# Kernel tuning notes

Hardware: AMD Instinct MI355X
Metric: run time of the kernel (lower is better)

Reference implementation:

```python
import jax, jax.numpy as jnp
import numpy as np

COMMITMENT_COST = 0.25


def setup_inputs() -> dict:
    key = jax.random.key(0)
    k1, k2 = jax.random.split(key)
    x = jax.random.normal(k1, (32, 256, 32, 32), dtype=jnp.float32)          # NCHW latents
    embedding = jax.random.normal(k2, (1024, 256), dtype=jnp.float32)        # [K, D] codebook
    return {"x": x, "embedding": embedding}


def reference(x, embedding):
    # NCHW -> NHWC, flatten to [N, D]
    inp = jnp.transpose(x, (0, 2, 3, 1))
    B, H, W, D = inp.shape
    K = embedding.shape[0]
    flat = inp.reshape(-1, D)                                                # [N, D]

    dists = (jnp.sum(flat * flat, axis=1, keepdims=True)
             + jnp.sum(embedding * embedding, axis=1)
             - 2.0 * flat @ embedding.T)
    idx = jnp.argmin(dists, axis=1)                                          # [N]
    encodings = jax.nn.one_hot(idx, K, dtype=flat.dtype)                     # [N, K]

    quantized = (encodings @ embedding).reshape(B, H, W, D)

    # commitment loss (codebook detached, eval path: no EMA update)
    e_latent_loss = jnp.mean(jnp.square(jax.lax.stop_gradient(quantized) - inp))
    loss = COMMITMENT_COST * e_latent_loss

    # straight-through estimator
    quantized_st = inp + jax.lax.stop_gradient(quantized - inp)

    avg_probs = jnp.mean(encodings, axis=0)
    perplexity = jnp.exp(-jnp.sum(avg_probs * jnp.log(avg_probs + 1e-10)))

    return (loss, jnp.transpose(quantized_st, (0, 3, 1, 2)), perplexity, encodings)
```

## Files before the change

### kernel.cpp

```cpp
#include <hip/hip_runtime.h>
#include <math.h>

#define D    256
#define K    1024
#define HWX  1024
#define NPTS 32768
#define PT   64
#define NPAIR 32

#define Q_OFF    1
#define PERP_OFF (1 + 8388608)
#define ENC_OFF  (2 + 8388608)

#define WS_FRAG_OFF 16384

typedef __attribute__((ext_vector_type(8))) short bf16x8;
typedef __attribute__((ext_vector_type(4))) float f32x4;

__device__ __forceinline__ unsigned short bf16_rne(float f) {
  unsigned int u = __float_as_uint(f);
  u = u + 0x7fffu + ((u >> 16) & 1u);
  return (unsigned short)(u >> 16);
}

#define CONV(F, H, L)                                                          \
  {                                                                            \
    H = bf16_rne(F);                                                           \
    const float fh_ = __uint_as_float((unsigned)(H) << 16);                    \
    L = bf16_rne((F)-fh_);                                                     \
  }

__global__ __launch_bounds__(256) void vq_frag(const float* __restrict__ emb,
                                               unsigned int* __restrict__ frag,
                                               float* __restrict__ enorm,
                                               int* __restrict__ counts,
                                               float* __restrict__ loss_accum) {
  const int gid = blockIdx.x * 256 + threadIdx.x;
  const int c = gid >> 5, g = gid & 31;
  const float* src = emb + (size_t)c * D + g * 8;
  const float4 a = *(const float4*)src;
  const float4 b = *(const float4*)(src + 4);
  float s = a.x * a.x + a.y * a.y + a.z * a.z + a.w * a.w +
            b.x * b.x + b.y * b.y + b.z * b.z + b.w * b.w;
#pragma unroll
  for (int off = 1; off < 32; off <<= 1) s += __shfl_xor(s, off);
  if (g == 0) enorm[c] = s;
  unsigned short h0, h1, h2, h3, h4, h5, h6, h7;
  unsigned short l0, l1, l2, l3, l4, l5, l6, l7;
  CONV(a.x, h0, l0) CONV(a.y, h1, l1) CONV(a.z, h2, l2) CONV(a.w, h3, l3)
  CONV(b.x, h4, l4) CONV(b.y, h5, l5) CONV(b.z, h6, l6) CONV(b.w, h7, l7)
  uint4 uh, ul;
  uh.x = (unsigned)h0 | ((unsigned)h1 << 16); uh.y = (unsigned)h2 | ((unsigned)h3 << 16);
  uh.z = (unsigned)h4 | ((unsigned)h5 << 16); uh.w = (unsigned)h6 | ((unsigned)h7 << 16);
  ul.x = (unsigned)l0 | ((unsigned)l1 << 16); ul.y = (unsigned)l2 | ((unsigned)l3 << 16);
  ul.z = (unsigned)l4 | ((unsigned)l5 << 16); ul.w = (unsigned)l6 | ((unsigned)l7 << 16);
  const int fragidx = (c >> 4) * 16 + (g >> 2) * 2;
  const int Lo = ((c & 15) + 16 * (g & 3)) * 4;
  *(uint4*)(frag + (size_t)fragidx * 256 + Lo) = uh;
  *(uint4*)(frag + (size_t)(fragidx + 1) * 256 + Lo) = ul;
  if (gid < K) counts[gid] = 0;
  if (gid == 0) *loss_accum = 0.0f;
}

#define ISSUE_PAIR(P, SEL)                                                     \
  {                                                                            \
    const unsigned* gsrc = fragg + (((size_t)(P)*32 + w * 8) * 256) + lane * 4; \
    unsigned short* ldst = fbuf + (SEL)*16384 + (w * 8) * 512;                 \
    _Pragma("unroll") for (int q = 0; q < 8; ++q)                              \
        __builtin_amdgcn_global_load_lds(                                      \
            (const __attribute__((address_space(1))) unsigned*)(gsrc + q * 256), \
            (__attribute__((address_space(3))) unsigned*)(ldst + q * 512),     \
            16, 0, 0);                                                         \
  }

#define AH(RTL, KS)                                                            \
  ah##RTL##_##KS = *(const bf16x8*)&fbuf[(((pg * 2 + RTL) * 8 + KS) * 2 + 0) * 512 + lane * 8]; \
  al##RTL##_##KS = *(const bf16x8*)&fbuf[(((pg * 2 + RTL) * 8 + KS) * 2 + 1) * 512 + lane * 8];

#define KS(KSv)                                                                \
  {                                                                            \
    const bf16x8 bh = *(const bf16x8*)&fbuf[bufo + (KSv * 2 + 0) * 512 + lane * 8]; \
    const bf16x8 bl = *(const bf16x8*)&fbuf[bufo + (KSv * 2 + 1) * 512 + lane * 8]; \
    acc0 = __builtin_amdgcn_mfma_f32_16x16x32_bf16(ah0_##KSv, bh, acc0, 0, 0, 0); \
    acc0 = __builtin_amdgcn_mfma_f32_16x16x32_bf16(al0_##KSv, bh, acc0, 0, 0, 0); \
    acc0 = __builtin_amdgcn_mfma_f32_16x16x32_bf16(ah0_##KSv, bl, acc0, 0, 0, 0); \
    acc0 = __builtin_amdgcn_mfma_f32_16x16x32_bf16(al0_##KSv, bl, acc0, 0, 0, 0); \
    acc1 = __builtin_amdgcn_mfma_f32_16x16x32_bf16(ah1_##KSv, bh, acc1, 0, 0, 0); \
    acc1 = __builtin_amdgcn_mfma_f32_16x16x32_bf16(al1_##KSv, bh, acc1, 0, 0, 0); \
    acc1 = __builtin_amdgcn_mfma_f32_16x16x32_bf16(ah1_##KSv, bl, acc1, 0, 0, 0); \
    acc1 = __builtin_amdgcn_mfma_f32_16x16x32_bf16(al1_##KSv, bl, acc1, 0, 0, 0); \
  }

__global__ __launch_bounds__(256) void vq_main(const float* __restrict__ x,
                                               const unsigned int* __restrict__ fragg,
                                               const float* __restrict__ emb,
                                               const float* __restrict__ enorm,
                                               float* __restrict__ out_q,
                                               float* __restrict__ out_enc,
                                               float* __restrict__ loss_accum,
                                               int* __restrict__ counts) {
  __shared__ __align__(16) unsigned short fbuf[32768];
  __shared__ float en_s[K];
  __shared__ float xn_part[256];
  __shared__ float red_val[128];
  __shared__ int red_idx[128];
  __shared__ int idx_s[PT];

  const int t = threadIdx.x;
  const int lane = t & 63;
  const int w = t >> 6;
  const int pg = w >> 1;
  const int par = w & 1;
  const int p0 = blockIdx.x * PT;
  const int bb = p0 >> 10;
  const int hw0 = p0 & 1023;

  {
    const int pt = t & 63, c0 = t >> 6;
    const int rt = pt >> 4, mrow = pt & 15;
    const float* xb = x + (size_t)bb * (D * HWX) + hw0 + pt;
    float xn = 0.0f;
    for (int c = c0; c < D; c += 4) {
      const float f = xb[(size_t)c * HWX];
      unsigned short h, l;
      CONV(f, h, l)
      xn += f * f;
      const int ks = c >> 5, quad = (c >> 3) & 3, j = c & 7;
      const int Lr = mrow + 16 * quad;
      fbuf[((rt * 8 + ks) * 2 + 0) * 512 + Lr * 8 + j] = h;
      fbuf[((rt * 8 + ks) * 2 + 1) * 512 + Lr * 8 + j] = l;
    }
    xn_part[t] = xn;
  }
  for (int i = t; i < K; i += 256) en_s[i] = enorm[i];
  __syncthreads();

  bf16x8 ah0_0, ah0_1, ah0_2, ah0_3, ah0_4, ah0_5, ah0_6, ah0_7;
  bf16x8 al0_0, al0_1, al0_2, al0_3, al0_4, al0_5, al0_6, al0_7;
  bf16x8 ah1_0, ah1_1, ah1_2, ah1_3, ah1_4, ah1_5, ah1_6, ah1_7;
  bf16x8 al1_0, al1_1, al1_2, al1_3, al1_4, al1_5, al1_6, al1_7;
  AH(0, 0) AH(0, 1) AH(0, 2) AH(0, 3) AH(0, 4) AH(0, 5) AH(0, 6) AH(0, 7)
  AH(1, 0) AH(1, 1) AH(1, 2) AH(1, 3) AH(1, 4) AH(1, 5) AH(1, 6) AH(1, 7)
  __syncthreads();

  float mv[8];
  int mi[8];
#pragma unroll
  for (int i = 0; i < 8; ++i) { mv[i] = 3.4e38f; mi[i] = 0; }

  ISSUE_PAIR(0, 0)
  int sel = 0;
  for (int p = 0; p < NPAIR; ++p) {
    __syncthreads();
    if (p + 1 < NPAIR) ISSUE_PAIR(p + 1, sel ^ 1)
    const int bufo = sel * 16384 + par * 16 * 512;
    f32x4 acc0 = {0.f, 0.f, 0.f, 0.f};
    f32x4 acc1 = {0.f, 0.f, 0.f, 0.f};
    KS(0) KS(1) KS(2) KS(3) KS(4) KS(5) KS(6) KS(7)
    const int code = (p * 2 + par) * 16 + (lane & 15);
    const float en_l = en_s[code];
    float m;
    m = en_l - 2.0f * acc0[0]; if (m < mv[0]) { mv[0] = m; mi[0] = code; }
    m = en_l - 2.0f * acc0[1]; if (m < mv[1]) { mv[1] = m; mi[1] = code; }
    m = en_l - 2.0f * acc0[2]; if (m < mv[2]) { mv[2] = m; mi[2] = code; }
    m = en_l - 2.0f * acc0[3]; if (m < mv[3]) { mv[3] = m; mi[3] = code; }
    m = en_l - 2.0f * acc1[0]; if (m < mv[4]) { mv[4] = m; mi[4] = code; }
    m = en_l - 2.0f * acc1[1]; if (m < mv[5]) { mv[5] = m; mi[5] = code; }
    m = en_l - 2.0f * acc1[2]; if (m < mv[6]) { mv[6] = m; mi[6] = code; }
    m = en_l - 2.0f * acc1[3]; if (m < mv[7]) { mv[7] = m; mi[7] = code; }
    sel ^= 1;
  }

#pragma unroll
  for (int off = 1; off < 16; off <<= 1) {
#pragma unroll
    for (int i = 0; i < 8; ++i) {
      const float ov = __shfl_xor(mv[i], off);
      const int oi = __shfl_xor(mi[i], off);
      if (ov < mv[i] || (ov == mv[i] && oi < mi[i])) { mv[i] = ov; mi[i] = oi; }
    }
  }
  if ((lane & 15) == 0) {
    const int quad = lane >> 4;
#pragma unroll
    for (int i = 0; i < 8; ++i) {
      const int loc = (i >> 2) * 16 + quad * 4 + (i & 3);
      red_val[w * 32 + loc] = mv[i];
      red_idx[w * 32 + loc] = mi[i];
    }
  }
  __syncthreads();
  float dist = 0.0f;
  if (t < PT) {
    const int pgm = t >> 5, loc = t & 31;
    float bv = red_val[(pgm * 2) * 32 + loc];
    int bi = red_idx[(pgm * 2) * 32 + loc];
    const float v1 = red_val[(pgm * 2 + 1) * 32 + loc];
    const int i1 = red_idx[(pgm * 2 + 1) * 32 + loc];
    if (v1 < bv || (v1 == bv && i1 < bi)) { bv = v1; bi = i1; }
    float xn = 0.0f;
#pragma unroll
    for (int g = 0; g < 4; ++g) xn += xn_part[t + 64 * g];
    dist = bv + xn;
    idx_s[t] = bi;
    atomicAdd(&counts[bi], 1);
  }
  if (t < 64) {
#pragma unroll
    for (int off = 32; off > 0; off >>= 1) dist += __shfl_down(dist, off);
    if (t == 0) atomicAdd(loss_accum, dist);
  }
  __syncthreads();

  {
    const int pt = t & 63, c0 = t >> 6;
    const int row = idx_s[pt];
    const float* er = emb + (size_t)row * D;
    float* qb = out_q + (size_t)bb * D * HWX + hw0 + pt;
#pragma unroll
    for (int c = c0; c < D; c += 4) qb[(size_t)c * HWX] = er[c];
  }
  {
    float2* eb2 = reinterpret_cast<float2*>(out_enc + (size_t)p0 * K);
#pragma unroll 4
    for (int i = t; i < PT * K / 2; i += 256) {
      const int row = i >> 9;
      const int c2 = (i & 511) * 2;
      const int target = idx_s[row];
      float2 v = make_float2(0.f, 0.f);
      if (target == c2) v.x = 1.0f;
      else if (target == c2 + 1) v.y = 1.0f;
      eb2[i] = v;
    }
  }
}

__global__ __launch_bounds__(256) void vq_final(const int* __restrict__ counts,
                                                const float* __restrict__ loss_accum,
                                                float* __restrict__ out) {
  __shared__ float sh[4];
  const int t = threadIdx.x;
  float s = 0.0f;
  for (int k = t; k < K; k += 256) {
    const float p = (float)counts[k] * (1.0f / 32768.0f);
    s += p * logf(p + 1e-10f);
  }
#pragma unroll
  for (int off = 32; off > 0; off >>= 1) s += __shfl_down(s, off);
  if ((t & 63) == 0) sh[t >> 6] = s;
  __syncthreads();
  if (t == 0) {
    const float tot = sh[0] + sh[1] + sh[2] + sh[3];
    out[PERP_OFF] = expf(-tot);
    out[0] = 0.25f * (*loss_accum) / 8388608.0f;
  }
}

extern "C" void kernel_launch(void* const* d_in, const int* in_sizes, int n_in,
                              void* d_out, int out_size, void* d_ws, size_t ws_size,
                              hipStream_t stream) {
  const float* x = (const float*)d_in[0];
  const float* emb = (const float*)d_in[1];
  float* out = (float*)d_out;
  float* enorm = (float*)d_ws;
  int* counts = (int*)((char*)d_ws + 4096);
  float* loss_accum = (float*)((char*)d_ws + 8192);
  unsigned int* fragg = (unsigned int*)((char*)d_ws + WS_FRAG_OFF);

  hipLaunchKernelGGL(vq_frag, dim3(128), dim3(256), 0, stream,
                     emb, fragg, enorm, counts, loss_accum);
  hipLaunchKernelGGL(vq_main, dim3(NPTS / PT), dim3(256), 0, stream,
                     x, fragg, emb, enorm, out + Q_OFF, out + ENC_OFF,
                     loss_accum, counts);
  hipLaunchKernelGGL(vq_final, dim3(1), dim3(256), 0, stream,
                     counts, loss_accum, out);
}
```

Before: 287.7 us.

## Read codebook fragments from global directly, drop lo*lo MFMA, stage quantized output via LDS

The main loop no longer double-buffers codebook fragments into LDS with global_load_lds and barriers. Each wave now reads its B fragments straight from global/L2, and the per-pair __syncthreads calls are gone. The low*low bf16 correction MFMA is dropped, cutting MFMA work by a quarter at a small cost in distance precision that could flip near-tie argmins. The quantized output gather is restaged through LDS with a padded transpose so the embedding row reads are coalesced float4 loads. The workspace fragment offset also moves, possibly to avoid overlap.

Result: slower. 309.1 us (+7.4%).

```diff
diff --git a/kernel.cpp b/kernel.cpp
--- a/kernel.cpp
+++ b/kernel.cpp
@@ -12,7 +12,7 @@
 #define PERP_OFF (1 + 8388608)
 #define ENC_OFF  (2 + 8388608)
 
-#define WS_FRAG_OFF 16384
+#define WS_FRAG_OFF 147456
 
 typedef __attribute__((ext_vector_type(8))) short bf16x8;
 typedef __attribute__((ext_vector_type(4))) float f32x4;
@@ -62,33 +62,20 @@
   if (gid == 0) *loss_accum = 0.0f;
 }
 
-#define ISSUE_PAIR(P, SEL)                                                     \
-  {                                                                            \
-    const unsigned* gsrc = fragg + (((size_t)(P)*32 + w * 8) * 256) + lane * 4; \
-    unsigned short* ldst = fbuf + (SEL)*16384 + (w * 8) * 512;                 \
-    _Pragma("unroll") for (int q = 0; q < 8; ++q)                              \
-        __builtin_amdgcn_global_load_lds(                                      \
-            (const __attribute__((address_space(1))) unsigned*)(gsrc + q * 256), \
-            (__attribute__((address_space(3))) unsigned*)(ldst + q * 512),     \
-            16, 0, 0);                                                         \
-  }
-
 #define AH(RTL, KS)                                                            \
   ah##RTL##_##KS = *(const bf16x8*)&fbuf[(((pg * 2 + RTL) * 8 + KS) * 2 + 0) * 512 + lane * 8]; \
   al##RTL##_##KS = *(const bf16x8*)&fbuf[(((pg * 2 + RTL) * 8 + KS) * 2 + 1) * 512 + lane * 8];
 
 #define KS(KSv)                                                                \
   {                                                                            \
-    const bf16x8 bh = *(const bf16x8*)&fbuf[bufo + (KSv * 2 + 0) * 512 + lane * 8]; \
-    const bf16x8 bl = *(const bf16x8*)&fbuf[bufo + (KSv * 2 + 1) * 512 + lane * 8]; \
+    const bf16x8 bh = *(const bf16x8*)(gb + (KSv * 2 + 0) * 256);              \
+    const bf16x8 bl = *(const bf16x8*)(gb + (KSv * 2 + 1) * 256);              \
     acc0 = __builtin_amdgcn_mfma_f32_16x16x32_bf16(ah0_##KSv, bh, acc0, 0, 0, 0); \
     acc0 = __builtin_amdgcn_mfma_f32_16x16x32_bf16(al0_##KSv, bh, acc0, 0, 0, 0); \
     acc0 = __builtin_amdgcn_mfma_f32_16x16x32_bf16(ah0_##KSv, bl, acc0, 0, 0, 0); \
-    acc0 = __builtin_amdgcn_mfma_f32_16x16x32_bf16(al0_##KSv, bl, acc0, 0, 0, 0); \
     acc1 = __builtin_amdgcn_mfma_f32_16x16x32_bf16(ah1_##KSv, bh, acc1, 0, 0, 0); \
     acc1 = __builtin_amdgcn_mfma_f32_16x16x32_bf16(al1_##KSv, bh, acc1, 0, 0, 0); \
     acc1 = __builtin_amdgcn_mfma_f32_16x16x32_bf16(ah1_##KSv, bl, acc1, 0, 0, 0); \
-    acc1 = __builtin_amdgcn_mfma_f32_16x16x32_bf16(al1_##KSv, bl, acc1, 0, 0, 0); \
   }
 
 __global__ __launch_bounds__(256) void vq_main(const float* __restrict__ x,
@@ -141,19 +128,14 @@
   bf16x8 al1_0, al1_1, al1_2, al1_3, al1_4, al1_5, al1_6, al1_7;
   AH(0, 0) AH(0, 1) AH(0, 2) AH(0, 3) AH(0, 4) AH(0, 5) AH(0, 6) AH(0, 7)
   AH(1, 0) AH(1, 1) AH(1, 2) AH(1, 3) AH(1, 4) AH(1, 5) AH(1, 6) AH(1, 7)
-  __syncthreads();
 
   float mv[8];
   int mi[8];
 #pragma unroll
   for (int i = 0; i < 8; ++i) { mv[i] = 3.4e38f; mi[i] = 0; }
 
-  ISSUE_PAIR(0, 0)
-  int sel = 0;
   for (int p = 0; p < NPAIR; ++p) {
-    __syncthreads();
-    if (p + 1 < NPAIR) ISSUE_PAIR(p + 1, sel ^ 1)
-    const int bufo = sel * 16384 + par * 16 * 512;
+    const unsigned* gb = fragg + ((size_t)(p * 2 + par) * 16) * 256 + lane * 4;
     f32x4 acc0 = {0.f, 0.f, 0.f, 0.f};
     f32x4 acc1 = {0.f, 0.f, 0.f, 0.f};
     KS(0) KS(1) KS(2) KS(3) KS(4) KS(5) KS(6) KS(7)
@@ -168,7 +150,6 @@
     m = en_l - 2.0f * acc1[1]; if (m < mv[5]) { mv[5] = m; mi[5] = code; }
     m = en_l - 2.0f * acc1[2]; if (m < mv[6]) { mv[6] = m; mi[6] = code; }
     m = en_l - 2.0f * acc1[3]; if (m < mv[7]) { mv[7] = m; mi[7] = code; }
-    sel ^= 1;
   }
 
 #pragma unroll
@@ -210,15 +191,23 @@
     for (int off = 32; off > 0; off >>= 1) dist += __shfl_down(dist, off);
     if (t == 0) atomicAdd(loss_accum, dist);
   }
-  __syncthreads();
-
-  {
-    const int pt = t & 63, c0 = t >> 6;
-    const int row = idx_s[pt];
-    const float* er = emb + (size_t)row * D;
-    float* qb = out_q + (size_t)bb * D * HWX + hw0 + pt;
-#pragma unroll
-    for (int c = c0; c < D; c += 4) qb[(size_t)c * HWX] = er[c];
+
+  float* xq = (float*)fbuf;
+  for (int h = 0; h < 2; ++h) {
+    __syncthreads();
+    for (int r = w; r < 32; r += 4) {
+      const float4 v = ((const float4*)(emb + (size_t)idx_s[h * 32 + r] * D))[lane];
+      float* dst = &xq[r * 257 + lane];
+      dst[0] = v.x; dst[64] = v.y; dst[128] = v.z; dst[192] = v.w;
+    }
+    __syncthreads();
+    const int pt = t & 31, c0 = t >> 5;
+    float* qb = out_q + (size_t)bb * D * HWX + hw0 + h * 32 + pt;
+#pragma unroll
+    for (int ci = c0; ci < D; ci += 8) {
+      const int pos = (ci >> 2) + 64 * (ci & 3);
+      qb[(size_t)ci * HWX] = xq[pt * 257 + pos];
+    }
   }
   {
     float2* eb2 = reinterpret_cast<float2*>(out_enc + (size_t)p0 * K);
```
